# Optimization experiments

Hardware: AMD Instinct MI355X
Metric: run time of the kernel (lower is better)

## Reference

```python
import jax, jax.numpy as jnp
import numpy as np

NOOBJ_LAMBDA = 0.5
COORD_LAMBDA = 5.0


def _cxcywh_to_xyxy(b):
    cx, cy, w, h = b[..., 0], b[..., 1], b[..., 2], b[..., 3]
    return jnp.stack([cx - w / 2, cy - h / 2, cx + w / 2, cy + h / 2], axis=-1)


def _pairwise_iou(a, b):
    # a: [B, N, 4] xyxy (preds), b: [B, M, 4] xyxy (targets) -> [B, N, M]
    lt = jnp.maximum(a[:, :, None, :2], b[:, None, :, :2])
    rb = jnp.minimum(a[:, :, None, 2:], b[:, None, :, 2:])
    wh = jnp.clip(rb - lt, 0.0)
    inter = wh[..., 0] * wh[..., 1]
    area_a = (a[..., 2] - a[..., 0]) * (a[..., 3] - a[..., 1])
    area_b = (b[..., 2] - b[..., 0]) * (b[..., 3] - b[..., 1])
    union = area_a[:, :, None] + area_b[:, None, :] - inter
    return inter / jnp.where(union > 0, union, 1.0)


def setup_inputs() -> dict:
    key = jax.random.key(0)
    kp, kt, km = jax.random.split(key, 3)
    B = 8192
    # positive values so sqrt(w), sqrt(h) is well-defined (as the torch code assumes)
    pred = jax.random.uniform(kp, (B, 7, 7, 30), dtype=jnp.float32, minval=0.05, maxval=1.0)
    target = jax.random.uniform(kt, (B, 7, 7, 30), dtype=jnp.float32, minval=0.05, maxval=1.0)
    # target confidence channel (index 4) is the obj/noobj indicator: 0 or 1
    obj = (jax.random.uniform(km, (B, 7, 7)) < 0.2).astype(jnp.float32)
    target = target.at[..., 4].set(obj)
    return {"pred_tensor": pred, "target_tensor": target}


def reference(pred_tensor, target_tensor):
    B = pred_tensor.shape[0]
    pred = pred_tensor.reshape(B, 49, 30)
    target = target_tensor.reshape(B, 49, 30)

    conf_t = target[..., 4]            # [B,49]
    noobj = conf_t == 0                # [B,49]
    obj = conf_t > 0                   # [B,49]

    # --- no-object confidence loss (channels 4 and 9) ---
    d4 = pred[..., 4] - target[..., 4]
    d9 = pred[..., 9] - target[..., 9]
    noobj_loss = jnp.sum(jnp.where(noobj, d4 * d4 + d9 * d9, 0.0))

    # --- object cells: 2 boxes per cell, padded to all 49 cells with a mask ---
    pb = pred[..., :10].reshape(B, 98, 5)
    tb = target[..., :10].reshape(B, 98, 5)
    box_mask = jnp.repeat(obj, 2, axis=1)  # [B,98]

    p_xyxy = _cxcywh_to_xyxy(pb[..., :4])
    t_xyxy = _cxcywh_to_xyxy(tb[..., :4])
    iou = _pairwise_iou(p_xyxy, t_xyxy)  # [B,98,98]
    pair_mask = box_mask[:, :, None] & box_mask[:, None, :]
    iou = jnp.where(pair_mask, iou, 0.0)
    max_iou = jnp.max(iou, axis=1)       # max over pred boxes, per target box [B,98]
    cmask = (max_iou != 0) & box_mask    # [B,98]

    cm = cmask.astype(pred.dtype)
    # coord (cx,cy) loss
    dxy = pb[..., :2] - tb[..., :2]
    coord_loss_cxcy = jnp.sum(cm * jnp.sum(dxy * dxy, axis=-1))
    # coord (sqrt w, sqrt h) loss
    dwh = jnp.sqrt(pb[..., 2:4]) - jnp.sqrt(tb[..., 2:4])
    coord_loss_wh = jnp.sum(cm * jnp.sum(dwh * dwh, axis=-1))
    # object confidence loss
    dconf = pb[..., 4] - tb[..., 4]
    obj_loss = jnp.sum(cm * dconf * dconf)

    # --- class loss over object cells ---
    dcls = pred[..., 10:] - target[..., 10:]
    cls_loss = jnp.sum(obj.astype(pred.dtype) * jnp.sum(dcls * dcls, axis=-1))

    bsz = jnp.asarray(B, pred.dtype)
    batch_cls_loss = cls_loss / bsz
    batch_obj_loss = (obj_loss + noobj_loss * NOOBJ_LAMBDA) / bsz
    batch_coord_loss = (coord_loss_cxcy + coord_loss_wh) * COORD_LAMBDA / bsz
    batch_loss = batch_cls_loss + batch_obj_loss + batch_coord_loss
    return (batch_loss, batch_cls_loss, batch_obj_loss, batch_coord_loss)
```

## Files before the change

### kernel.cpp

```cpp
#include <hip/hip_runtime.h>

#define CH 30
#define CELLS 49
#define ROWF 1470
#define WPB 4

__device__ __forceinline__ float waveReduce(float v) {
    #pragma unroll
    for (int o = 32; o > 0; o >>= 1) v += __shfl_xor(v, o, 64);
    return v;
}

__global__ __launch_bounds__(256) void yolo_main(const float* __restrict__ pred,
                                                 const float* __restrict__ targ,
                                                 float* __restrict__ ws, int B,
                                                 int NB) {
    const int w = threadIdx.x >> 6;
    const int lane = threadIdx.x & 63;
    const int r = blockIdx.x * WPB + w;

    __shared__ float4 boxS[WPB][2 * CELLS];
    __shared__ int clist[WPB][CELLS];
    __shared__ float sred[WPB][3];

    float cls = 0.f, objc = 0.f, coord = 0.f;

    if (r < B) {
        const float* P = pred + (size_t)r * ROWF;
        const float* T = targ + (size_t)r * ROWF;

        const int cl = lane < CELLS ? lane : CELLS - 1;
        const float t4 = T[cl * CH + 4];
        const float p4 = P[cl * CH + 4];
        const float t9 = T[cl * CH + 9];
        const float p9 = P[cl * CH + 9];

        const bool act = lane < CELLS;
        const bool isObj = act && (t4 > 0.f);
        const unsigned long long m = __ballot(isObj);

        if (act && !isObj) {
            const float d4 = p4 - t4, d9 = p9 - t9;
            objc += 0.5f * (d4 * d4 + d9 * d9);
        }

        const int nObj = __popcll(m);
        if (isObj) clist[w][__popcll(m & ((1ull << lane) - 1ull))] = lane;

        if (nObj) {
            const int nBox = 2 * nObj;
            const int nCls = nObj * 20;

            int cidx[4]; float cp[4], ct[4];
            #pragma unroll
            for (int j = 0; j < 4; ++j) {
                const int idx = lane + j * 64;
                const int ic = idx < nCls ? idx : nCls - 1;
                cidx[j] = idx;
                const int cc = (ic * 3277) >> 16;
                const int ch = 10 + (ic - cc * 20);
                const int c = clist[w][cc];
                cp[j] = P[c * CH + ch];
                ct[j] = T[c * CH + ch];
            }
            const int e0 = lane, e1 = lane + 64;
            const int c0 = clist[w][(e0 < nBox ? e0 : 0) >> 1];
            const int c1 = clist[w][(e1 < nBox ? e1 : 0) >> 1];
            const int b0 = c0 * CH + (e0 & 1) * 5;
            const int b1 = c1 * CH + (e1 & 1) * 5;
            const float4 pB0 = *(const float4*)(P + b0);
            const float4 tB0 = *(const float4*)(T + b0);
            const float pE0 = P[b0 + 4], tE0 = T[b0 + 4];
            const float4 pB1 = *(const float4*)(P + b1);
            const float4 tB1 = *(const float4*)(T + b1);
            const float pE1 = P[b1 + 4], tE1 = T[b1 + 4];

            #pragma unroll
            for (int j = 0; j < 4; ++j) {
                const float dv = cp[j] - ct[j];
                cls += (cidx[j] < nCls) ? dv * dv : 0.f;
            }
            for (int base = 256; base < nCls; base += 64) {
                const int idx = base + lane;
                if (idx < nCls) {
                    const int cc = (idx * 3277) >> 16;
                    const int ch = 10 + (idx - cc * 20);
                    const int c = clist[w][cc];
                    const float dv = P[c * CH + ch] - T[c * CH + ch];
                    cls += dv * dv;
                }
            }

            if (e0 < nBox)
                boxS[w][e0] = make_float4(pB0.x - 0.5f * pB0.z, pB0.y - 0.5f * pB0.w,
                                          pB0.x + 0.5f * pB0.z, pB0.y + 0.5f * pB0.w);
            if (e1 < nBox)
                boxS[w][e1] = make_float4(pB1.x - 0.5f * pB1.z, pB1.y - 0.5f * pB1.w,
                                          pB1.x + 0.5f * pB1.z, pB1.y + 0.5f * pB1.w);

            #pragma unroll
            for (int eh = 0; eh < 2; ++eh) {
                const int e = eh ? e1 : e0;
                if (e < nBox) {
                    const float4 tb = eh ? tB1 : tB0;
                    const float4 pb = eh ? pB1 : pB0;
                    const float pe = eh ? pE1 : pE0;
                    const float te = eh ? tE1 : tE0;
                    const float tx1 = tb.x - 0.5f * tb.z, ty1 = tb.y - 0.5f * tb.w;
                    const float tx2 = tb.x + 0.5f * tb.z, ty2 = tb.y + 0.5f * tb.w;
                    const float ta = (tx2 - tx1) * (ty2 - ty1);
                    float maxiou = 0.f;
                    for (int i = 0; i < nBox; ++i) {
                        const float4 pb4 = boxS[w][i];
                        const float lx = fmaxf(pb4.x, tx1), ly = fmaxf(pb4.y, ty1);
                        const float rx = fminf(pb4.z, tx2), ry = fminf(pb4.w, ty2);
                        const float iw = fmaxf(rx - lx, 0.f), ih = fmaxf(ry - ly, 0.f);
                        const float inter = iw * ih;
                        const float pa = (pb4.z - pb4.x) * (pb4.w - pb4.y);
                        const float un = pa + ta - inter;
                        const float iou = inter / (un > 0.f ? un : 1.f);
                        maxiou = fmaxf(maxiou, iou);
                    }
                    if (maxiou != 0.f) {
                        const float dcx = pb.x - tb.x, dcy = pb.y - tb.y;
                        coord += dcx * dcx + dcy * dcy;
                        const float dw = sqrtf(pb.z) - sqrtf(tb.z);
                        const float dh = sqrtf(pb.w) - sqrtf(tb.w);
                        coord += dw * dw + dh * dh;
                        const float dc = pe - te;
                        objc += dc * dc;
                    }
                }
            }
        }
    }

    cls = waveReduce(cls); objc = waveReduce(objc); coord = waveReduce(coord);
    if (lane == 0) { sred[w][0] = cls; sred[w][1] = objc; sred[w][2] = coord; }
    __syncthreads();
    if (threadIdx.x == 0) {
        float C = 0.f, O = 0.f, X = 0.f;
        #pragma unroll
        for (int k = 0; k < WPB; ++k) { C += sred[k][0]; O += sred[k][1]; X += sred[k][2]; }
        ws[blockIdx.x] = C;
        ws[NB + blockIdx.x] = O;
        ws[2 * NB + blockIdx.x] = X;
    }
}

__global__ __launch_bounds__(1024) void yolo_reduce(const float* __restrict__ ws,
                                                    float* __restrict__ out,
                                                    int NB, float invB) {
    const int tid = threadIdx.x;
    const int w = tid >> 6, lane = tid & 63;
    float c = 0.f, o = 0.f, x = 0.f;
    for (int i = tid; i < NB; i += 1024) {
        c += ws[i];
        o += ws[NB + i];
        x += ws[2 * NB + i];
    }
    c = waveReduce(c); o = waveReduce(o); x = waveReduce(x);
    __shared__ float sred[16][3];
    if (lane == 0) { sred[w][0] = c; sred[w][1] = o; sred[w][2] = x; }
    __syncthreads();
    if (tid == 0) {
        float C = 0.f, O = 0.f, X = 0.f;
        #pragma unroll
        for (int k = 0; k < 16; ++k) { C += sred[k][0]; O += sred[k][1]; X += sred[k][2]; }
        const float bcls = C * invB;
        const float bobj = O * invB;
        const float bcoord = X * 5.0f * invB;
        out[0] = bcls + bobj + bcoord;
        out[1] = bcls;
        out[2] = bobj;
        out[3] = bcoord;
    }
}

extern "C" void kernel_launch(void* const* d_in, const int* in_sizes, int n_in,
                              void* d_out, int out_size, void* d_ws, size_t ws_size,
                              hipStream_t stream) {
    const float* pred = (const float*)d_in[0];
    const float* targ = (const float*)d_in[1];
    float* ws = (float*)d_ws;
    float* out = (float*)d_out;
    const int B = in_sizes[0] / ROWF;
    const int NB = (B + WPB - 1) / WPB;

    yolo_main<<<NB, 256, 0, stream>>>(pred, targ, ws, B, NB);
    yolo_reduce<<<1, 1024, 0, stream>>>(ws, out, NB, 1.0f / (float)B);
}
```

Before: 122.0 us.

## Stream class loss with coalesced float4 loads across block rows using object masks

```diff
diff --git a/kernel.cpp b/kernel.cpp
--- a/kernel.cpp
+++ b/kernel.cpp
@@ -3,6 +3,7 @@
 #define CH 30
 #define CELLS 49
 #define ROWF 1470
+#define RPB 4
 #define WPB 4
 
 __device__ __forceinline__ float waveReduce(float v) {
@@ -17,119 +18,134 @@
                                                  int NB) {
     const int w = threadIdx.x >> 6;
     const int lane = threadIdx.x & 63;
-    const int r = blockIdx.x * WPB + w;
-
+    const int r0 = blockIdx.x * RPB;
+    const int myrow = r0 + w;
+    const int nrows = (B - r0) < RPB ? (B - r0) : RPB;
+
+    __shared__ unsigned long long lmask[RPB];
     __shared__ float4 boxS[WPB][2 * CELLS];
     __shared__ int clist[WPB][CELLS];
     __shared__ float sred[WPB][3];
 
     float cls = 0.f, objc = 0.f, coord = 0.f;
-
-    if (r < B) {
-        const float* P = pred + (size_t)r * ROWF;
-        const float* T = targ + (size_t)r * ROWF;
-
+    unsigned long long mymask = 0ull;
+
+    if (w < nrows) {
+        const float* P = pred + (size_t)myrow * ROWF;
+        const float* T = targ + (size_t)myrow * ROWF;
         const int cl = lane < CELLS ? lane : CELLS - 1;
         const float t4 = T[cl * CH + 4];
         const float p4 = P[cl * CH + 4];
         const float t9 = T[cl * CH + 9];
         const float p9 = P[cl * CH + 9];
-
         const bool act = lane < CELLS;
         const bool isObj = act && (t4 > 0.f);
-        const unsigned long long m = __ballot(isObj);
-
+        mymask = __ballot(isObj);
         if (act && !isObj) {
             const float d4 = p4 - t4, d9 = p9 - t9;
             objc += 0.5f * (d4 * d4 + d9 * d9);
         }
-
-        const int nObj = __popcll(m);
-        if (isObj) clist[w][__popcll(m & ((1ull << lane) - 1ull))] = lane;
-
-        if (nObj) {
-            const int nBox = 2 * nObj;
-            const int nCls = nObj * 20;
-
-            int cidx[4]; float cp[4], ct[4];
+        if (lane == 0) lmask[w] = mymask;
+    } else if (w < RPB && lane == 0) {
+        lmask[w] = 0ull;
+    }
+    __syncthreads();
+
+    {
+        const float4* Pb = (const float4*)(pred + (size_t)r0 * ROWF);
+        const float4* Tb = (const float4*)(targ + (size_t)r0 * ROWF);
+        const int npair = nrows * 735;
+        const int nq4 = npair >> 1;
+        for (int i = threadIdx.x; i < nq4; i += 256) {
+            const float4 pv = Pb[i];
+            const float4 tv = Tb[i];
             #pragma unroll
-            for (int j = 0; j < 4; ++j) {
-                const int idx = lane + j * 64;
-                const int ic = idx < nCls ? idx : nCls - 1;
-                cidx[j] = idx;
-                const int cc = (ic * 3277) >> 16;
-                const int ch = 10 + (ic - cc * 20);
-                const int c = clist[w][cc];
-                cp[j] = P[c * CH + ch];
-                ct[j] = T[c * CH + ch];
+            for (int k = 0; k < 2; ++k) {
+                const int p = 2 * i + k;
+                const int rl = (p * 5707) >> 22;
+                const int pr = p - rl * 735;
+                const int cell = (pr * 17477) >> 18;
+                const int ch0 = 2 * (pr - cell * 15);
+                const unsigned long long mk = lmask[rl];
+                const float wobj = (float)((mk >> cell) & 1ull);
+                const float dx = (k ? pv.z : pv.x) - (k ? tv.z : tv.x);
+                const float dy = (k ? pv.w : pv.y) - (k ? tv.w : tv.y);
+                cls += (ch0 >= 10) ? wobj * (dx * dx + dy * dy) : 0.f;
             }
-            const int e0 = lane, e1 = lane + 64;
-            const int c0 = clist[w][(e0 < nBox ? e0 : 0) >> 1];
-            const int c1 = clist[w][(e1 < nBox ? e1 : 0) >> 1];
-            const int b0 = c0 * CH + (e0 & 1) * 5;
-            const int b1 = c1 * CH + (e1 & 1) * 5;
-            const float4 pB0 = *(const float4*)(P + b0);
-            const float4 tB0 = *(const float4*)(T + b0);
-            const float pE0 = P[b0 + 4], tE0 = T[b0 + 4];
-            const float4 pB1 = *(const float4*)(P + b1);
-            const float4 tB1 = *(const float4*)(T + b1);
-            const float pE1 = P[b1 + 4], tE1 = T[b1 + 4];
-
-            #pragma unroll
-            for (int j = 0; j < 4; ++j) {
-                const float dv = cp[j] - ct[j];
-                cls += (cidx[j] < nCls) ? dv * dv : 0.f;
+        }
+        if (npair & 1) {
+            const int p = npair - 1;
+            if (threadIdx.x == 0) {
+                const int rl = (p * 5707) >> 22;
+                const int pr = p - rl * 735;
+                const int cell = (pr * 17477) >> 18;
+                const int ch0 = 2 * (pr - cell * 15);
+                const float* Pf = pred + (size_t)r0 * ROWF + 2 * p;
+                const float* Tf = targ + (size_t)r0 * ROWF + 2 * p;
+                const float wobj = (float)((lmask[rl] >> cell) & 1ull);
+                const float dx = Pf[0] - Tf[0], dy = Pf[1] - Tf[1];
+                cls += (ch0 >= 10) ? wobj * (dx * dx + dy * dy) : 0.f;
             }
-            for (int base = 256; base < nCls; base += 64) {
-                const int idx = base + lane;
-                if (idx < nCls) {
-                    const int cc = (idx * 3277) >> 16;
-                    const int ch = 10 + (idx - cc * 20);
-                    const int c = clist[w][cc];
-                    const float dv = P[c * CH + ch] - T[c * CH + ch];
-                    cls += dv * dv;
+        }
+    }
+
+    if (w < nrows && mymask) {
+        const float* P = pred + (size_t)myrow * ROWF;
+        const float* T = targ + (size_t)myrow * ROWF;
+        const int nBox = 2 * __popcll(mymask);
+        const bool isObj = (lane < CELLS) && ((mymask >> lane) & 1ull);
+        if (isObj) clist[w][__popcll(mymask & ((1ull << lane) - 1ull))] = lane;
+
+        const int e0 = lane, e1 = lane + 64;
+        const int c0 = clist[w][(e0 < nBox ? e0 : 0) >> 1];
+        const int c1 = clist[w][(e1 < nBox ? e1 : 0) >> 1];
+        const int b0 = c0 * CH + (e0 & 1) * 5;
+        const int b1 = c1 * CH + (e1 & 1) * 5;
+        const float4 pB0 = *(const float4*)(P + b0);
+        const float4 tB0 = *(const float4*)(T + b0);
+        const float pE0 = P[b0 + 4], tE0 = T[b0 + 4];
+        const float4 pB1 = *(const float4*)(P + b1);
+        const float4 tB1 = *(const float4*)(T + b1);
+        const float pE1 = P[b1 + 4], tE1 = T[b1 + 4];
+
+        if (e0 < nBox)
+            boxS[w][e0] = make_float4(pB0.x - 0.5f * pB0.z, pB0.y - 0.5f * pB0.w,
+                                      pB0.x + 0.5f * pB0.z, pB0.y + 0.5f * pB0.w);
+        if (e1 < nBox)
+            boxS[w][e1] = make_float4(pB1.x - 0.5f * pB1.z, pB1.y - 0.5f * pB1.w,
+                                      pB1.x + 0.5f * pB1.z, pB1.y + 0.5f * pB1.w);
+
+        #pragma unroll
+        for (int eh = 0; eh < 2; ++eh) {
+            const int e = eh ? e1 : e0;
+            if (e < nBox) {
+                const float4 tb = eh ? tB1 : tB0;
+                const float4 pb = eh ? pB1 : pB0;
+                const float pe = eh ? pE1 : pE0;
+                const float te = eh ? tE1 : tE0;
+                const float tx1 = tb.x - 0.5f * tb.z, ty1 = tb.y - 0.5f * tb.w;
+                const float tx2 = tb.x + 0.5f * tb.z, ty2 = tb.y + 0.5f * tb.w;
+                const float ta = (tx2 - tx1) * (ty2 - ty1);
+                float maxiou = 0.f;
+                for (int i = 0; i < nBox; ++i) {
+                    const float4 pb4 = boxS[w][i];
+                    const float lx = fmaxf(pb4.x, tx1), ly = fmaxf(pb4.y, ty1);
+                    const float rx = fminf(pb4.z, tx2), ry = fminf(pb4.w, ty2);
+                    const float iw = fmaxf(rx - lx, 0.f), ih = fmaxf(ry - ly, 0.f);
+                    const float inter = iw * ih;
+                    const float pa = (pb4.z - pb4.x) * (pb4.w - pb4.y);
+                    const float un = pa + ta - inter;
+                    const float iou = inter / (un > 0.f ? un : 1.f);
+                    maxiou = fmaxf(maxiou, iou);
                 }
-            }
-
-            if (e0 < nBox)
-                boxS[w][e0] = make_float4(pB0.x - 0.5f * pB0.z, pB0.y - 0.5f * pB0.w,
-                                          pB0.x + 0.5f * pB0.z, pB0.y + 0.5f * pB0.w);
-            if (e1 < nBox)
-                boxS[w][e1] = make_float4(pB1.x - 0.5f * pB1.z, pB1.y - 0.5f * pB1.w,
-                                          pB1.x + 0.5f * pB1.z, pB1.y + 0.5f * pB1.w);
-
-            #pragma unroll
-            for (int eh = 0; eh < 2; ++eh) {
-                const int e = eh ? e1 : e0;
-                if (e < nBox) {
-                    const float4 tb = eh ? tB1 : tB0;
-                    const float4 pb = eh ? pB1 : pB0;
-                    const float pe = eh ? pE1 : pE0;
-                    const float te = eh ? tE1 : tE0;
-                    const float tx1 = tb.x - 0.5f * tb.z, ty1 = tb.y - 0.5f * tb.w;
-                    const float tx2 = tb.x + 0.5f * tb.z, ty2 = tb.y + 0.5f * tb.w;
-                    const float ta = (tx2 - tx1) * (ty2 - ty1);
-                    float maxiou = 0.f;
-                    for (int i = 0; i < nBox; ++i) {
-                        const float4 pb4 = boxS[w][i];
-                        const float lx = fmaxf(pb4.x, tx1), ly = fmaxf(pb4.y, ty1);
-                        const float rx = fminf(pb4.z, tx2), ry = fminf(pb4.w, ty2);
-                        const float iw = fmaxf(rx - lx, 0.f), ih = fmaxf(ry - ly, 0.f);
-                        const float inter = iw * ih;
-                        const float pa = (pb4.z - pb4.x) * (pb4.w - pb4.y);
-                        const float un = pa + ta - inter;
-                        const float iou = inter / (un > 0.f ? un : 1.f);
-                        maxiou = fmaxf(maxiou, iou);
-                    }
-                    if (maxiou != 0.f) {
-                        const float dcx = pb.x - tb.x, dcy = pb.y - tb.y;
-                        coord += dcx * dcx + dcy * dcy;
-                        const float dw = sqrtf(pb.z) - sqrtf(tb.z);
-                        const float dh = sqrtf(pb.w) - sqrtf(tb.w);
-                        coord += dw * dw + dh * dh;
-                        const float dc = pe - te;
-                        objc += dc * dc;
-                    }
+                if (maxiou != 0.f) {
+                    const float dcx = pb.x - tb.x, dcy = pb.y - tb.y;
+                    coord += dcx * dcx + dcy * dcy;
+                    const float dw = sqrtf(pb.z) - sqrtf(tb.z);
+                    const float dh = sqrtf(pb.w) - sqrtf(tb.w);
+                    coord += dw * dw + dh * dh;
+                    const float dc = pe - te;
+                    objc += dc * dc;
                 }
             }
         }
@@ -185,7 +201,7 @@
     float* ws = (float*)d_ws;
     float* out = (float*)d_out;
     const int B = in_sizes[0] / ROWF;
-    const int NB = (B + WPB - 1) / WPB;
+    const int NB = (B + RPB - 1) / RPB;
 
     yolo_main<<<NB, 256, 0, stream>>>(pred, targ, ws, B, NB);
     yolo_reduce<<<1, 1024, 0, stream>>>(ws, out, NB, 1.0f / (float)B);
```

Measured after the change: 131.0 us. +7.4%, slower.
